# Performance work log

Hardware: AMD Instinct MI355X
Metric: run time of the kernel (lower is better)

## Reference

```python
import jax, jax.numpy as jnp
import numpy as np

B, N, C, K = 8, 2048, 512, 1


def setup_inputs() -> dict:
    key = jax.random.key(0)
    ks = jax.random.split(key, 10)
    s = 1.0 / np.sqrt(C)
    f32 = jnp.float32
    return {
        "x": jax.random.normal(ks[0], (B, N, C), f32),
        "neighbors": jax.random.randint(ks[1], (N, K), 0, N),
        "Wq": jax.random.normal(ks[2], (C, C), f32) * s,
        "bq": jnp.zeros((C,), f32),
        "Wk": jax.random.normal(ks[3], (C, C), f32) * s,
        "bk": jnp.zeros((C,), f32),
        "Wv": jax.random.normal(ks[4], (C, C), f32) * s,
        "bv": jnp.zeros((C,), f32),
        "rel_bias": jnp.zeros((K, K), f32),  # nn.Parameter(torch.zeros(k,k))
        "Wo": jax.random.normal(ks[5], (C, C), f32) * s,
        "bo": jnp.zeros((C,), f32),
    }


def reference(x, neighbors, Wq, bq, Wk, bk, Wv, bv, rel_bias, Wo, bo):
    # torch Linear: y = x @ W.T + b
    Q = jnp.einsum("bnc,dc->bnd", x, Wq) + bq
    Kt = jnp.einsum("bnc,dc->bnd", x, Wk) + bk
    V = jnp.einsum("bnc,dc->bnd", x, Wv) + bv

    nbr = neighbors[:, 0]  # [N], the single neighbor of each position (k==1)
    Kn = Kt[:, nbr, :]     # [B,N,C] gathered keys
    Vn = V[:, nbr, :]      # [B,N,C] gathered values (V_neighbors viewed as [B,N,k*C])

    # per-position score q_i . k_{nbr_i} + bias scalar
    s = jnp.einsum("bnc,bnc->bn", Q, Kn) + rel_bias[0, 0]

    # dense NxN score matrix, zeros elsewhere (faithful: softmax includes the zeros)
    scores = jnp.zeros((B, N, N), x.dtype).at[:, jnp.arange(N), nbr].set(s)
    probs = jax.nn.softmax(scores / jnp.asarray(np.sqrt(C), x.dtype), axis=-1)

    out = jnp.einsum("bnm,bmc->bnc", probs, Vn)
    return jnp.einsum("bnc,dc->bnd", out, Wo) + bo
```

## Files before the change

### kernel.cpp

```cpp
#include <hip/hip_runtime.h>
#include <hip/hip_bf16.h>
#include <math.h>

namespace {
constexpr int kB = 8;
constexpr int kN = 2048;
constexpr int kC = 512;
constexpr int kR = kB * kN;
constexpr int kNC = 2 * kC;
constexpr float kInvSqrtC = 0.044194173824159216f;

typedef __attribute__((ext_vector_type(8))) short short8;
typedef __attribute__((ext_vector_type(4))) short short4b;
typedef __attribute__((ext_vector_type(4))) float f32x4;
typedef unsigned short ushort;
}

static __device__ __forceinline__ float bf2f(ushort u) {
  union { unsigned int i; float f; } v; v.i = (unsigned int)u << 16; return v.f;
}
static __device__ __forceinline__ ushort f2bf(float f) {
  __hip_bfloat16 h = __float2bfloat16(f);
  union { __hip_bfloat16 h; ushort u; } cv; cv.h = h; return cv.u;
}

#define GLOAD16(G, L) __builtin_amdgcn_global_load_lds( \
    (const __attribute__((address_space(1))) unsigned int*)(G), \
    (__attribute__((address_space(3))) unsigned int*)(L), 16, 0, 0)

__global__ __launch_bounds__(256) void castw_kernel(
    const float* __restrict__ Wq, const float* __restrict__ Wk,
    const float* __restrict__ Wv, const float* __restrict__ Wo,
    ushort* __restrict__ WqT, ushort* __restrict__ WkT,
    ushort* __restrict__ WvT, ushort* __restrict__ Woh,
    const int* __restrict__ nbr, int* __restrict__ cnt) {
  const int z = blockIdx.z;
  const int t = threadIdx.x;
  if (z == 4) {
    if (blockIdx.x || blockIdx.y) return;
    __shared__ int h[kN];
#pragma unroll
    for (int i = 0; i < 8; i++) h[t + i * 256] = 0;
    __syncthreads();
#pragma unroll
    for (int i = 0; i < 8; i++) atomicAdd(&h[nbr[t + i * 256]], 1);
    __syncthreads();
#pragma unroll
    for (int i = 0; i < 8; i++) cnt[t + i * 256] = h[t + i * 256];
    return;
  }
  const int d0 = blockIdx.x * 64, c0 = blockIdx.y * 64;
  if (z == 3) {
#pragma unroll
    for (int i = 0; i < 4; i++) {
      const int row = i * 16 + (t >> 4), col4 = (t & 15) * 4;
      const float4 v = *reinterpret_cast<const float4*>(&Wo[(d0 + row) * kC + c0 + col4]);
      short4b o;
      o[0] = (short)f2bf(v.x); o[1] = (short)f2bf(v.y);
      o[2] = (short)f2bf(v.z); o[3] = (short)f2bf(v.w);
      *reinterpret_cast<short4b*>(&Woh[(d0 + row) * kC + c0 + col4]) = o;
    }
    return;
  }
  __shared__ float ld[64][65];
  const float* S = (z == 0) ? Wq : ((z == 1) ? Wk : Wv);
  ushort* T = (z == 0) ? WqT : ((z == 1) ? WkT : WvT);
#pragma unroll
  for (int i = 0; i < 4; i++) {
    const int dl = i * 16 + (t >> 4), cl4 = (t & 15) * 4;
    const float4 v = *reinterpret_cast<const float4*>(&S[(d0 + dl) * kC + c0 + cl4]);
    ld[dl][cl4 + 0] = v.x; ld[dl][cl4 + 1] = v.y;
    ld[dl][cl4 + 2] = v.z; ld[dl][cl4 + 3] = v.w;
  }
  __syncthreads();
#pragma unroll
  for (int i = 0; i < 4; i++) {
    const int cl = i * 16 + (t >> 4), dl4 = (t & 15) * 4;
    short4b o;
#pragma unroll
    for (int q = 0; q < 4; q++) o[q] = (short)f2bf(ld[dl4 + q][cl]);
    *reinterpret_cast<short4b*>(&T[(size_t)(c0 + cl) * kC + d0 + dl4]) = o;
  }
}

__global__ __launch_bounds__(256) void fold_kernel(
    const ushort* __restrict__ WqT, const ushort* __restrict__ WkT,
    const ushort* __restrict__ Woh, const ushort* __restrict__ WvT,
    ushort* __restrict__ Bh,
    const float* __restrict__ bq, const float* __restrict__ bk, const float* __restrict__ bv,
    float* __restrict__ biascat, float* __restrict__ vbq, float* __restrict__ bqbk) {
  const int t = threadIdx.x, lane = t & 63, w = t >> 6;
  const int z = blockIdx.z;
  if (z == 2) {
    const int fid = blockIdx.y * 8 + blockIdx.x;
    const int gw = fid * 4 + w;
    for (int rr = gw; rr < 1536; rr += 256) {
      const ushort* rowp; const float* vec;
      if (rr < 512)       { rowp = &WqT[(size_t)rr * kC];          vec = bk; }
      else if (rr < 1024) { rowp = &WkT[(size_t)(rr - 512) * kC];  vec = bq; }
      else                { rowp = &Woh[(size_t)(rr - 1024) * kC]; vec = bv; }
      const short8 u = *reinterpret_cast<const short8*>(&rowp[lane * 8]);
      const float4 v0 = *reinterpret_cast<const float4*>(&vec[lane * 8]);
      const float4 v1 = *reinterpret_cast<const float4*>(&vec[lane * 8 + 4]);
      float a = bf2f((ushort)u[0]) * v0.x + bf2f((ushort)u[1]) * v0.y +
                bf2f((ushort)u[2]) * v0.z + bf2f((ushort)u[3]) * v0.w +
                bf2f((ushort)u[4]) * v1.x + bf2f((ushort)u[5]) * v1.y +
                bf2f((ushort)u[6]) * v1.z + bf2f((ushort)u[7]) * v1.w;
#pragma unroll
      for (int off = 32; off; off >>= 1) a += __shfl_xor(a, off);
      if (lane == 0) {
        if (rr < 512) biascat[rr] = a;
        else if (rr < 1024) vbq[rr - 512] = a;
        else biascat[rr - 512] = a;
      }
    }
    if (gw == 0) {
      const float4 q0 = *reinterpret_cast<const float4*>(&bq[lane * 8]);
      const float4 q1 = *reinterpret_cast<const float4*>(&bq[lane * 8 + 4]);
      const float4 k0 = *reinterpret_cast<const float4*>(&bk[lane * 8]);
      const float4 k1 = *reinterpret_cast<const float4*>(&bk[lane * 8 + 4]);
      float s = q0.x * k0.x + q0.y * k0.y + q0.z * k0.z + q0.w * k0.w +
                q1.x * k1.x + q1.y * k1.y + q1.z * k1.z + q1.w * k1.w;
#pragma unroll
      for (int off = 32; off; off >>= 1) s += __shfl_xor(s, off);
      if (lane == 0) bqbk[0] = s;
    }
    return;
  }
  __shared__ ushort lA[64 * 64];
  __shared__ ushort lB[64 * 64];
  const ushort* Ap = z ? Woh : WqT;
  const ushort* Bp = z ? WvT : WkT;
  const int r0 = blockIdx.y * 64, c0 = blockIdx.x * 64;
  const int wr = (w >> 1) * 32, wc = (w & 1) * 32;
  const int srow = t >> 3, scol = (t & 7) * 8;
  f32x4 acc[2][2] = {};
  for (int k0 = 0; k0 < kC; k0 += 64) {
#pragma unroll
    for (int it = 0; it < 2; it++) {
      GLOAD16(&Ap[(size_t)(r0 + it * 32 + srow) * kC + k0 + scol], &lA[(it * 32 + srow) * 64 + scol]);
      GLOAD16(&Bp[(size_t)(c0 + it * 32 + srow) * kC + k0 + scol], &lB[(it * 32 + srow) * 64 + scol]);
    }
    __syncthreads();
#pragma unroll
    for (int kk = 0; kk < 2; kk++) {
      const int ko = kk * 32 + (lane >> 4) * 8;
      short8 af[2], bfr[2];
#pragma unroll
      for (int i = 0; i < 2; i++)
        af[i] = *reinterpret_cast<const short8*>(&lA[(wr + i * 16 + (lane & 15)) * 64 + ko]);
#pragma unroll
      for (int j = 0; j < 2; j++)
        bfr[j] = *reinterpret_cast<const short8*>(&lB[(wc + j * 16 + (lane & 15)) * 64 + ko]);
#pragma unroll
      for (int i = 0; i < 2; i++)
#pragma unroll
        for (int j = 0; j < 2; j++)
          acc[i][j] = __builtin_amdgcn_mfma_f32_16x16x32_bf16(af[i], bfr[j], acc[i][j], 0, 0, 0);
    }
    __syncthreads();
  }
#pragma unroll
  for (int j = 0; j < 2; j++) {
    const int col = c0 + wc + j * 16 + (lane & 15);
#pragma unroll
    for (int i = 0; i < 2; i++) {
      const int rbase = r0 + wr + i * 16 + (lane >> 4) * 4;
#pragma unroll
      for (int q = 0; q < 4; q++)
        Bh[(size_t)(z * kC + rbase + q) * kC + col] = f2bf(acc[i][j][q]);
    }
  }
}

__global__ __launch_bounds__(256) void castg_kernel(
    const float* __restrict__ x, const float* __restrict__ vbq,
    ushort* __restrict__ xh, float* __restrict__ g) {
  const int wid = threadIdx.x >> 6, lane = threadIdx.x & 63;
  const int r = blockIdx.x * 4 + wid;
  const float4 a = *reinterpret_cast<const float4*>(&x[(size_t)r * kC + lane * 8]);
  const float4 b = *reinterpret_cast<const float4*>(&x[(size_t)r * kC + lane * 8 + 4]);
  short8 o;
  o[0] = (short)f2bf(a.x); o[1] = (short)f2bf(a.y);
  o[2] = (short)f2bf(a.z); o[3] = (short)f2bf(a.w);
  o[4] = (short)f2bf(b.x); o[5] = (short)f2bf(b.y);
  o[6] = (short)f2bf(b.z); o[7] = (short)f2bf(b.w);
  *reinterpret_cast<short8*>(&xh[(size_t)r * kC + lane * 8]) = o;
  const float4 v0 = *reinterpret_cast<const float4*>(&vbq[lane * 8]);
  const float4 v1 = *reinterpret_cast<const float4*>(&vbq[lane * 8 + 4]);
  float acc = a.x * v0.x + a.y * v0.y + a.z * v0.z + a.w * v0.w +
              b.x * v1.x + b.y * v1.y + b.z * v1.z + b.w * v1.w;
#pragma unroll
  for (int off = 32; off; off >>= 1) acc += __shfl_xor(acc, off);
  if (lane == 0) g[r] = acc;
}

__global__ __launch_bounds__(256) void mm_kernel(
    const ushort* __restrict__ xh, const ushort* __restrict__ Bh,
    const float* __restrict__ biascat, const int* __restrict__ cnt,
    ushort* __restrict__ obuf, float* __restrict__ part2) {
  __shared__ ushort lA[2][128 * 64];
  __shared__ ushort lB[2][128 * 64];
  __shared__ float cs[2][128];
  const int id = blockIdx.x;
  const int orig = (id & 7) * 128 + (id >> 3);
  const int r0 = (orig >> 3) * 128;
  const int c0 = (orig & 7) * 128;
  const int t = threadIdx.x;
  const int lane = t & 63, w = t >> 6;
  const int wr = (w >> 1) * 64, wc = (w & 1) * 64;
  const int srow = t >> 3, scol = (t & 7) * 8;
  f32x4 acc[4][4] = {};

  auto stage = [&](int buf, int k0) {
#pragma unroll
    for (int it = 0; it < 4; it++) {
      GLOAD16(&xh[(size_t)(r0 + it * 32 + srow) * kC + k0 + scol],
              &lA[buf][(it * 32 + srow) * 64 + scol]);
      GLOAD16(&Bh[(size_t)(c0 + it * 32 + srow) * kC + k0 + scol],
              &lB[buf][(it * 32 + srow) * 64 + scol]);
    }
  };

  stage(0, 0);
  __syncthreads();
  int cur = 0;
#pragma unroll
  for (int ts = 0; ts < 8; ++ts) {
    if (ts < 7) stage(cur ^ 1, (ts + 1) * 64);
#pragma unroll
    for (int kk = 0; kk < 2; kk++) {
      const int ko = kk * 32 + (lane >> 4) * 8;
      short8 af[4], bfr[4];
#pragma unroll
      for (int i = 0; i < 4; i++)
        af[i] = *reinterpret_cast<const short8*>(&lA[cur][(wr + i * 16 + (lane & 15)) * 64 + ko]);
#pragma unroll
      for (int j = 0; j < 4; j++)
        bfr[j] = *reinterpret_cast<const short8*>(&lB[cur][(wc + j * 16 + (lane & 15)) * 64 + ko]);
      __builtin_amdgcn_s_setprio(1);
#pragma unroll
      for (int i = 0; i < 4; i++)
#pragma unroll
        for (int j = 0; j < 4; j++)
          acc[i][j] = __builtin_amdgcn_mfma_f32_16x16x32_bf16(af[i], bfr[j], acc[i][j], 0, 0, 0);
      __builtin_amdgcn_s_setprio(0);
    }
    __syncthreads();
    cur ^= 1;
  }

  const bool isVo = (c0 >= 512);
  float cw[4][4];
  if (isVo) {
    const int jb0 = (r0 & (kN - 1)) + wr + ((lane >> 4) << 2);
#pragma unroll
    for (int i = 0; i < 4; i++) {
      const int4 c4 = *reinterpret_cast<const int4*>(&cnt[jb0 + i * 16]);
      cw[i][0] = (float)c4.x; cw[i][1] = (float)c4.y;
      cw[i][2] = (float)c4.z; cw[i][3] = (float)c4.w;
    }
  }
  float psum[4] = {0.f, 0.f, 0.f, 0.f};
#pragma unroll
  for (int j = 0; j < 4; j++) {
    const int col = c0 + wc + j * 16 + (lane & 15);
    const float bias = biascat[col];
#pragma unroll
    for (int i = 0; i < 4; i++) {
      const int rbase = r0 + wr + i * 16 + (lane >> 4) * 4;
#pragma unroll
      for (int q = 0; q < 4; q++) {
        const float v = acc[i][j][q] + bias;
        obuf[(size_t)(rbase + q) * kNC + col] = f2bf(v);
        if (isVo) psum[j] += v * cw[i][q];
      }
    }
  }
  if (isVo) {
#pragma unroll
    for (int j = 0; j < 4; j++) {
      psum[j] += __shfl_xor(psum[j], 16);
      psum[j] += __shfl_xor(psum[j], 32);
    }
    if (lane < 16) {
#pragma unroll
      for (int j = 0; j < 4; j++) cs[w >> 1][wc + j * 16 + lane] = psum[j];
    }
    __syncthreads();
    if (t < 128) {
      const int b = r0 >> 11, rt = (r0 & (kN - 1)) >> 7;
      part2[(size_t)(b * 16 + rt) * kC + (c0 - 512) + t] = cs[0][t] + cs[1][t];
    }
  }
}

__global__ __launch_bounds__(256) void svo_reduce_kernel(
    const float* __restrict__ part2, float* __restrict__ svo) {
  const int d = blockIdx.x * 256 + threadIdx.x;
  const int b = blockIdx.y;
  float a = 0.f;
#pragma unroll
  for (int rt = 0; rt < 16; rt++) a += part2[(size_t)(b * 16 + rt) * kC + d];
  svo[b * kC + d] = a;
}

__global__ __launch_bounds__(256) void final_kernel(
    const ushort* __restrict__ xh, const ushort* __restrict__ obuf,
    const float* __restrict__ svo, const float* __restrict__ g, const int* __restrict__ nbr,
    const float* __restrict__ bqbk, const float* __restrict__ rb, const float* __restrict__ bo,
    float* __restrict__ out) {
  const int wid = threadIdx.x >> 6, lane = threadIdx.x & 63;
  const int rg = blockIdx.x * 4 + wid;
  const int b = rg >> 11, n = rg & (kN - 1);
  const int j = nbr[n];
  const int j2 = nbr[j];
  const short8 xv = *reinterpret_cast<const short8*>(&xh[(size_t)rg * kC + lane * 8]);
  const short8 wv = *reinterpret_cast<const short8*>(&obuf[(size_t)(b * kN + j) * kNC + lane * 8]);
  float a = 0.f;
#pragma unroll
  for (int q = 0; q < 8; q++) a += bf2f((ushort)xv[q]) * bf2f((ushort)wv[q]);
#pragma unroll
  for (int off = 32; off; off >>= 1) a += __shfl_xor(a, off);
  const float s = a + g[b * kN + j] + bqbk[0] + rb[0];
  const float tt = s * kInvSqrtC;
  const float e = expf(tt);
  const float inv = 1.0f / (e + (float)(kN - 1));
  const float coef = (e - 1.0f) * inv;
  const short8 vv = *reinterpret_cast<const short8*>(&obuf[(size_t)(b * kN + j2) * kNC + kC + lane * 8]);
  const float4 s0 = *reinterpret_cast<const float4*>(&svo[b * kC + lane * 8]);
  const float4 s1 = *reinterpret_cast<const float4*>(&svo[b * kC + lane * 8 + 4]);
  const float4 b0 = *reinterpret_cast<const float4*>(&bo[lane * 8]);
  const float4 b1 = *reinterpret_cast<const float4*>(&bo[lane * 8 + 4]);
  float4 r0, r1;
  r0.x = s0.x * inv + bf2f((ushort)vv[0]) * coef + b0.x;
  r0.y = s0.y * inv + bf2f((ushort)vv[1]) * coef + b0.y;
  r0.z = s0.z * inv + bf2f((ushort)vv[2]) * coef + b0.z;
  r0.w = s0.w * inv + bf2f((ushort)vv[3]) * coef + b0.w;
  r1.x = s1.x * inv + bf2f((ushort)vv[4]) * coef + b1.x;
  r1.y = s1.y * inv + bf2f((ushort)vv[5]) * coef + b1.y;
  r1.z = s1.z * inv + bf2f((ushort)vv[6]) * coef + b1.z;
  r1.w = s1.w * inv + bf2f((ushort)vv[7]) * coef + b1.w;
  *reinterpret_cast<float4*>(&out[(size_t)rg * kC + lane * 8]) = r0;
  *reinterpret_cast<float4*>(&out[(size_t)rg * kC + lane * 8 + 4]) = r1;
}

extern "C" void kernel_launch(void* const* d_in, const int* in_sizes, int n_in,
                              void* d_out, int out_size, void* d_ws, size_t ws_size,
                              hipStream_t stream) {
  const float* x  = (const float*)d_in[0];
  const int* nbr  = (const int*)d_in[1];
  const float* Wq = (const float*)d_in[2];
  const float* bq = (const float*)d_in[3];
  const float* Wk = (const float*)d_in[4];
  const float* bk = (const float*)d_in[5];
  const float* Wv = (const float*)d_in[6];
  const float* bv = (const float*)d_in[7];
  const float* rb = (const float*)d_in[8];
  const float* Wo = (const float*)d_in[9];
  const float* bo = (const float*)d_in[10];
  float* out = (float*)d_out;

  char* ws = (char*)d_ws;
  size_t off = 0;
  auto alloc = [&](size_t bytes) -> void* {
    void* p = ws + off;
    off = (off + bytes + 255) & ~(size_t)255;
    return p;
  };
  ushort* xh    = (ushort*)alloc((size_t)kR * kC * 2);
  ushort* Bh    = (ushort*)alloc((size_t)kNC * kC * 2);
  ushort* obuf  = (ushort*)alloc((size_t)kR * kNC * 2);
  ushort* WqT   = (ushort*)alloc((size_t)kC * kC * 2);
  ushort* WkT   = (ushort*)alloc((size_t)kC * kC * 2);
  ushort* WvT   = (ushort*)alloc((size_t)kC * kC * 2);
  ushort* Woh   = (ushort*)alloc((size_t)kC * kC * 2);
  float* biascat = (float*)alloc(kNC * 4);
  float* vbq    = (float*)alloc(kC * 4);
  float* bqbk   = (float*)alloc(4);
  int*   cnt    = (int*)alloc(kN * 4);
  float* g      = (float*)alloc((size_t)kR * 4);
  float* svo    = (float*)alloc((size_t)kB * kC * 4);
  float* part2  = (float*)alloc((size_t)kB * 16 * kC * 4);
  (void)ws_size; (void)n_in; (void)in_sizes; (void)out_size;

  castw_kernel<<<dim3(8, 8, 5), 256, 0, stream>>>(Wq, Wk, Wv, Wo, WqT, WkT, WvT, Woh, nbr, cnt);
  fold_kernel<<<dim3(8, 8, 3), 256, 0, stream>>>(WqT, WkT, Woh, WvT, Bh, bq, bk, bv, biascat, vbq, bqbk);
  castg_kernel<<<kR / 4, 256, 0, stream>>>(x, vbq, xh, g);
  mm_kernel<<<1024, 256, 0, stream>>>(xh, Bh, biascat, cnt, obuf, part2);
  svo_reduce_kernel<<<dim3(2, kB), 256, 0, stream>>>(part2, svo);
  final_kernel<<<kR / 4, 256, 0, stream>>>(xh, obuf, svo, g, nbr, bqbk, rb, bo, out);
}
```

Before: 70.86 us.

## Merge x cast into prep kernel, stage GEMM epilogue through LDS, fuse aux reductions

The x-to-bf16 cast moves into the weight-prep launch as extra grid slices, so it can run before the weight fold. The g dot product is recomputed from bf16 xh inside a new aux kernel that also does the svo reduction, removing one launch. The mm epilogue now writes fp32 tiles to reused LDS and then emits coalesced 16-byte bf16 stores instead of scattered 2-byte stores. The cost is an extra LDS round trip and a barrier in the epilogue, and g now carries slightly lower precision because it is computed from bf16 inputs.

Result: slower. 72.36 us (+2.1%).

```diff
diff --git a/kernel.cpp b/kernel.cpp
--- a/kernel.cpp
+++ b/kernel.cpp
@@ -28,17 +28,33 @@
     (const __attribute__((address_space(1))) unsigned int*)(G), \
     (__attribute__((address_space(3))) unsigned int*)(L), 16, 0, 0)
 
-__global__ __launch_bounds__(256) void castw_kernel(
+__global__ __launch_bounds__(256) void prep_kernel(
     const float* __restrict__ Wq, const float* __restrict__ Wk,
     const float* __restrict__ Wv, const float* __restrict__ Wo,
     ushort* __restrict__ WqT, ushort* __restrict__ WkT,
     ushort* __restrict__ WvT, ushort* __restrict__ Woh,
-    const int* __restrict__ nbr, int* __restrict__ cnt) {
+    const int* __restrict__ nbr, int* __restrict__ cnt,
+    const float* __restrict__ x, ushort* __restrict__ xh) {
+  __shared__ __align__(16) char sm[64 * 65 * 4];
   const int z = blockIdx.z;
   const int t = threadIdx.x;
+  if (z >= 5) {
+    const int wid = t >> 6, lane = t & 63;
+    const int bid = blockIdx.y * 8 + blockIdx.x;
+    const int r = ((z - 5) * 64 + bid) * 4 + wid;
+    const float4 a = *reinterpret_cast<const float4*>(&x[(size_t)r * kC + lane * 8]);
+    const float4 b = *reinterpret_cast<const float4*>(&x[(size_t)r * kC + lane * 8 + 4]);
+    short8 o;
+    o[0] = (short)f2bf(a.x); o[1] = (short)f2bf(a.y);
+    o[2] = (short)f2bf(a.z); o[3] = (short)f2bf(a.w);
+    o[4] = (short)f2bf(b.x); o[5] = (short)f2bf(b.y);
+    o[6] = (short)f2bf(b.z); o[7] = (short)f2bf(b.w);
+    *reinterpret_cast<short8*>(&xh[(size_t)r * kC + lane * 8]) = o;
+    return;
+  }
   if (z == 4) {
     if (blockIdx.x || blockIdx.y) return;
-    __shared__ int h[kN];
+    int* h = (int*)sm;
 #pragma unroll
     for (int i = 0; i < 8; i++) h[t + i * 256] = 0;
     __syncthreads();
@@ -62,7 +78,7 @@
     }
     return;
   }
-  __shared__ float ld[64][65];
+  float (*ld)[65] = (float(*)[65])sm;
   const float* S = (z == 0) ? Wq : ((z == 1) ? Wk : Wv);
   ushort* T = (z == 0) ? WqT : ((z == 1) ? WkT : WvT);
 #pragma unroll
@@ -173,35 +189,14 @@
   }
 }
 
-__global__ __launch_bounds__(256) void castg_kernel(
-    const float* __restrict__ x, const float* __restrict__ vbq,
-    ushort* __restrict__ xh, float* __restrict__ g) {
-  const int wid = threadIdx.x >> 6, lane = threadIdx.x & 63;
-  const int r = blockIdx.x * 4 + wid;
-  const float4 a = *reinterpret_cast<const float4*>(&x[(size_t)r * kC + lane * 8]);
-  const float4 b = *reinterpret_cast<const float4*>(&x[(size_t)r * kC + lane * 8 + 4]);
-  short8 o;
-  o[0] = (short)f2bf(a.x); o[1] = (short)f2bf(a.y);
-  o[2] = (short)f2bf(a.z); o[3] = (short)f2bf(a.w);
-  o[4] = (short)f2bf(b.x); o[5] = (short)f2bf(b.y);
-  o[6] = (short)f2bf(b.z); o[7] = (short)f2bf(b.w);
-  *reinterpret_cast<short8*>(&xh[(size_t)r * kC + lane * 8]) = o;
-  const float4 v0 = *reinterpret_cast<const float4*>(&vbq[lane * 8]);
-  const float4 v1 = *reinterpret_cast<const float4*>(&vbq[lane * 8 + 4]);
-  float acc = a.x * v0.x + a.y * v0.y + a.z * v0.z + a.w * v0.w +
-              b.x * v1.x + b.y * v1.y + b.z * v1.z + b.w * v1.w;
-#pragma unroll
-  for (int off = 32; off; off >>= 1) acc += __shfl_xor(acc, off);
-  if (lane == 0) g[r] = acc;
-}
-
 __global__ __launch_bounds__(256) void mm_kernel(
     const ushort* __restrict__ xh, const ushort* __restrict__ Bh,
     const float* __restrict__ biascat, const int* __restrict__ cnt,
     ushort* __restrict__ obuf, float* __restrict__ part2) {
-  __shared__ ushort lA[2][128 * 64];
-  __shared__ ushort lB[2][128 * 64];
-  __shared__ float cs[2][128];
+  __shared__ __align__(16) char smem[68608];
+  ushort* lds = (ushort*)smem;
+  float* fbuf = (float*)smem;
+  float* cs = (float*)(smem + 67584);
   const int id = blockIdx.x;
   const int orig = (id & 7) * 128 + (id >> 3);
   const int r0 = (orig >> 3) * 128;
@@ -216,9 +211,9 @@
 #pragma unroll
     for (int it = 0; it < 4; it++) {
       GLOAD16(&xh[(size_t)(r0 + it * 32 + srow) * kC + k0 + scol],
-              &lA[buf][(it * 32 + srow) * 64 + scol]);
+              lds + buf * 8192 + (it * 32 + srow) * 64 + scol);
       GLOAD16(&Bh[(size_t)(c0 + it * 32 + srow) * kC + k0 + scol],
-              &lB[buf][(it * 32 + srow) * 64 + scol]);
+              lds + 16384 + buf * 8192 + (it * 32 + srow) * 64 + scol);
     }
   };
 
@@ -234,10 +229,10 @@
       short8 af[4], bfr[4];
 #pragma unroll
       for (int i = 0; i < 4; i++)
-        af[i] = *reinterpret_cast<const short8*>(&lA[cur][(wr + i * 16 + (lane & 15)) * 64 + ko]);
+        af[i] = *reinterpret_cast<const short8*>(&lds[cur * 8192 + (wr + i * 16 + (lane & 15)) * 64 + ko]);
 #pragma unroll
       for (int j = 0; j < 4; j++)
-        bfr[j] = *reinterpret_cast<const short8*>(&lB[cur][(wc + j * 16 + (lane & 15)) * 64 + ko]);
+        bfr[j] = *reinterpret_cast<const short8*>(&lds[16384 + cur * 8192 + (wc + j * 16 + (lane & 15)) * 64 + ko]);
       __builtin_amdgcn_s_setprio(1);
 #pragma unroll
       for (int i = 0; i < 4; i++)
@@ -261,18 +256,20 @@
       cw[i][2] = (float)c4.z; cw[i][3] = (float)c4.w;
     }
   }
+  float bias[4];
+#pragma unroll
+  for (int j = 0; j < 4; j++) bias[j] = biascat[c0 + wc + j * 16 + (lane & 15)];
   float psum[4] = {0.f, 0.f, 0.f, 0.f};
 #pragma unroll
   for (int j = 0; j < 4; j++) {
-    const int col = c0 + wc + j * 16 + (lane & 15);
-    const float bias = biascat[col];
+    const int lcol = wc + j * 16 + (lane & 15);
 #pragma unroll
     for (int i = 0; i < 4; i++) {
-      const int rbase = r0 + wr + i * 16 + (lane >> 4) * 4;
+      const int lrow = wr + i * 16 + (lane >> 4) * 4;
 #pragma unroll
       for (int q = 0; q < 4; q++) {
-        const float v = acc[i][j][q] + bias;
-        obuf[(size_t)(rbase + q) * kNC + col] = f2bf(v);
+        const float v = acc[i][j][q] + bias[j];
+        fbuf[(lrow + q) * 132 + lcol] = v;
         if (isVo) psum[j] += v * cw[i][q];
       }
     }
@@ -285,24 +282,56 @@
     }
     if (lane < 16) {
 #pragma unroll
-      for (int j = 0; j < 4; j++) cs[w >> 1][wc + j * 16 + lane] = psum[j];
-    }
-    __syncthreads();
-    if (t < 128) {
-      const int b = r0 >> 11, rt = (r0 & (kN - 1)) >> 7;
-      part2[(size_t)(b * 16 + rt) * kC + (c0 - 512) + t] = cs[0][t] + cs[1][t];
-    }
-  }
-}
-
-__global__ __launch_bounds__(256) void svo_reduce_kernel(
-    const float* __restrict__ part2, float* __restrict__ svo) {
-  const int d = blockIdx.x * 256 + threadIdx.x;
-  const int b = blockIdx.y;
-  float a = 0.f;
-#pragma unroll
-  for (int rt = 0; rt < 16; rt++) a += part2[(size_t)(b * 16 + rt) * kC + d];
-  svo[b * kC + d] = a;
+      for (int j = 0; j < 4; j++) cs[(w >> 1) * 128 + wc + j * 16 + lane] = psum[j];
+    }
+  }
+  __syncthreads();
+  {
+    const int rr = t >> 1, h = t & 1;
+    const size_t grow = (size_t)(r0 + rr);
+#pragma unroll
+    for (int s = 0; s < 8; s++) {
+      const float4 a4 = *reinterpret_cast<const float4*>(&fbuf[rr * 132 + h * 64 + s * 8]);
+      const float4 b4 = *reinterpret_cast<const float4*>(&fbuf[rr * 132 + h * 64 + s * 8 + 4]);
+      short8 o;
+      o[0] = (short)f2bf(a4.x); o[1] = (short)f2bf(a4.y);
+      o[2] = (short)f2bf(a4.z); o[3] = (short)f2bf(a4.w);
+      o[4] = (short)f2bf(b4.x); o[5] = (short)f2bf(b4.y);
+      o[6] = (short)f2bf(b4.z); o[7] = (short)f2bf(b4.w);
+      *reinterpret_cast<short8*>(&obuf[grow * kNC + c0 + h * 64 + s * 8]) = o;
+    }
+  }
+  if (isVo && t < 128) {
+    const int b = r0 >> 11, rt = (r0 & (kN - 1)) >> 7;
+    part2[(size_t)(b * 16 + rt) * kC + (c0 - 512) + t] = cs[t] + cs[128 + t];
+  }
+}
+
+__global__ __launch_bounds__(256) void aux_kernel(
+    const float* __restrict__ part2, float* __restrict__ svo,
+    const ushort* __restrict__ xh, const float* __restrict__ vbq, float* __restrict__ g) {
+  const int bx = blockIdx.x;
+  if (bx < 16) {
+    const int d = (bx & 1) * 256 + threadIdx.x;
+    const int b = bx >> 1;
+    float a = 0.f;
+#pragma unroll
+    for (int rt = 0; rt < 16; rt++) a += part2[(size_t)(b * 16 + rt) * kC + d];
+    svo[b * kC + d] = a;
+    return;
+  }
+  const int wid = threadIdx.x >> 6, lane = threadIdx.x & 63;
+  const int r = (bx - 16) * 4 + wid;
+  const short8 u = *reinterpret_cast<const short8*>(&xh[(size_t)r * kC + lane * 8]);
+  const float4 v0 = *reinterpret_cast<const float4*>(&vbq[lane * 8]);
+  const float4 v1 = *reinterpret_cast<const float4*>(&vbq[lane * 8 + 4]);
+  float a = bf2f((ushort)u[0]) * v0.x + bf2f((ushort)u[1]) * v0.y +
+            bf2f((ushort)u[2]) * v0.z + bf2f((ushort)u[3]) * v0.w +
+            bf2f((ushort)u[4]) * v1.x + bf2f((ushort)u[5]) * v1.y +
+            bf2f((ushort)u[6]) * v1.z + bf2f((ushort)u[7]) * v1.w;
+#pragma unroll
+  for (int off = 32; off; off >>= 1) a += __shfl_xor(a, off);
+  if (lane == 0) g[r] = a;
 }
 
 __global__ __launch_bounds__(256) void final_kernel(
@@ -384,10 +413,9 @@
   float* part2  = (float*)alloc((size_t)kB * 16 * kC * 4);
   (void)ws_size; (void)n_in; (void)in_sizes; (void)out_size;
 
-  castw_kernel<<<dim3(8, 8, 5), 256, 0, stream>>>(Wq, Wk, Wv, Wo, WqT, WkT, WvT, Woh, nbr, cnt);
+  prep_kernel<<<dim3(8, 8, 69), 256, 0, stream>>>(Wq, Wk, Wv, Wo, WqT, WkT, WvT, Woh, nbr, cnt, x, xh);
   fold_kernel<<<dim3(8, 8, 3), 256, 0, stream>>>(WqT, WkT, Woh, WvT, Bh, bq, bk, bv, biascat, vbq, bqbk);
-  castg_kernel<<<kR / 4, 256, 0, stream>>>(x, vbq, xh, g);
   mm_kernel<<<1024, 256, 0, stream>>>(xh, Bh, biascat, cnt, obuf, part2);
-  svo_reduce_kernel<<<dim3(2, kB), 256, 0, stream>>>(part2, svo);
+  aux_kernel<<<16 + kR / 4, 256, 0, stream>>>(part2, svo, xh, vbq, g);
   final_kernel<<<kR / 4, 256, 0, stream>>>(xh, obuf, svo, g, nbr, bqbk, rb, bo, out);
 }
```

## Compact GEMM rows to referenced neighbor positions and skip unused row tiles

Applied to the files above, without the earlier changes.

The neighbor histogram kernel now also builds a compacted list of positions that are referenced at least once, with their counts. The main GEMM gathers A rows through this list, scatters outputs back to the original rows, and exits early for row tiles beyond the compacted count (writing zero partial sums). With random neighbors only about 63% of positions are referenced, so roughly a third of GEMM tiles can be skipped. The cost is a serial-ish prefix scan in one block, indirect row loads and scattered stores. Rows of obuf that are never referenced are left unwritten, so correctness depends on final_kernel only reading referenced rows.

Measured after the change: 67.99 us, median of 2. 4.0% less time.

```diff
diff --git a/kernel.cpp b/kernel.cpp
--- a/kernel.cpp
+++ b/kernel.cpp
@@ -33,12 +33,14 @@
     const float* __restrict__ Wv, const float* __restrict__ Wo,
     ushort* __restrict__ WqT, ushort* __restrict__ WkT,
     ushort* __restrict__ WvT, ushort* __restrict__ Woh,
-    const int* __restrict__ nbr, int* __restrict__ cnt) {
+    const int* __restrict__ nbr, int* __restrict__ cnt,
+    int* __restrict__ jlist, int* __restrict__ cnt_c, int* __restrict__ meta) {
   const int z = blockIdx.z;
   const int t = threadIdx.x;
   if (z == 4) {
     if (blockIdx.x || blockIdx.y) return;
     __shared__ int h[kN];
+    __shared__ int wsum[256];
 #pragma unroll
     for (int i = 0; i < 8; i++) h[t + i * 256] = 0;
     __syncthreads();
@@ -47,6 +49,30 @@
     __syncthreads();
 #pragma unroll
     for (int i = 0; i < 8; i++) cnt[t + i * 256] = h[t + i * 256];
+    const int base = t * 8;
+    int lpre[8], lc = 0;
+#pragma unroll
+    for (int i = 0; i < 8; i++) { lpre[i] = lc; lc += (h[base + i] > 0) ? 1 : 0; }
+    wsum[t] = lc;
+    __syncthreads();
+    for (int off = 1; off < 256; off <<= 1) {
+      const int v = (t >= off) ? wsum[t - off] : 0;
+      __syncthreads();
+      wsum[t] += v;
+      __syncthreads();
+    }
+    const int excl = (t == 0) ? 0 : wsum[t - 1];
+    const int total = wsum[255];
+#pragma unroll
+    for (int i = 0; i < 8; i++) {
+      if (h[base + i] > 0) {
+        const int p = excl + lpre[i];
+        jlist[p] = base + i;
+        cnt_c[p] = h[base + i];
+      }
+    }
+    for (int p = total + t; p < kN; p += 256) { jlist[p] = 0; cnt_c[p] = 0; }
+    if (t == 0) meta[0] = total;
     return;
   }
   const int d0 = blockIdx.x * 64, c0 = blockIdx.y * 64;
@@ -197,25 +223,36 @@
 
 __global__ __launch_bounds__(256) void mm_kernel(
     const ushort* __restrict__ xh, const ushort* __restrict__ Bh,
-    const float* __restrict__ biascat, const int* __restrict__ cnt,
+    const float* __restrict__ biascat,
+    const int* __restrict__ cnt_c, const int* __restrict__ jlist, const int* __restrict__ meta,
     ushort* __restrict__ obuf, float* __restrict__ part2) {
   __shared__ ushort lA[2][128 * 64];
   __shared__ ushort lB[2][128 * 64];
   __shared__ float cs[2][128];
   const int id = blockIdx.x;
   const int orig = (id & 7) * 128 + (id >> 3);
-  const int r0 = (orig >> 3) * 128;
+  const int rt = orig >> 3;
   const int c0 = (orig & 7) * 128;
+  const int b = rt >> 4, lt = rt & 15;
   const int t = threadIdx.x;
+  const bool isVo = (c0 >= 512);
+  if (lt * 128 >= meta[0]) {
+    if (isVo && t < 128)
+      part2[(size_t)(b * 16 + lt) * kC + (c0 - 512) + t] = 0.f;
+    return;
+  }
   const int lane = t & 63, w = t >> 6;
   const int wr = (w >> 1) * 64, wc = (w & 1) * 64;
   const int srow = t >> 3, scol = (t & 7) * 8;
+  int jl[4];
+#pragma unroll
+  for (int it = 0; it < 4; it++) jl[it] = jlist[lt * 128 + it * 32 + srow];
   f32x4 acc[4][4] = {};
 
   auto stage = [&](int buf, int k0) {
 #pragma unroll
     for (int it = 0; it < 4; it++) {
-      GLOAD16(&xh[(size_t)(r0 + it * 32 + srow) * kC + k0 + scol],
+      GLOAD16(&xh[(size_t)(b * kN + jl[it]) * kC + k0 + scol],
               &lA[buf][(it * 32 + srow) * 64 + scol]);
       GLOAD16(&Bh[(size_t)(c0 + it * 32 + srow) * kC + k0 + scol],
               &lB[buf][(it * 32 + srow) * 64 + scol]);
@@ -250,13 +287,18 @@
     cur ^= 1;
   }
 
-  const bool isVo = (c0 >= 512);
+  const int cbase = lt * 128 + wr + ((lane >> 4) << 2);
   float cw[4][4];
+  int rj[4][4];
+#pragma unroll
+  for (int i = 0; i < 4; i++) {
+    const int4 j4 = *reinterpret_cast<const int4*>(&jlist[cbase + i * 16]);
+    rj[i][0] = j4.x; rj[i][1] = j4.y; rj[i][2] = j4.z; rj[i][3] = j4.w;
+  }
   if (isVo) {
-    const int jb0 = (r0 & (kN - 1)) + wr + ((lane >> 4) << 2);
 #pragma unroll
     for (int i = 0; i < 4; i++) {
-      const int4 c4 = *reinterpret_cast<const int4*>(&cnt[jb0 + i * 16]);
+      const int4 c4 = *reinterpret_cast<const int4*>(&cnt_c[cbase + i * 16]);
       cw[i][0] = (float)c4.x; cw[i][1] = (float)c4.y;
       cw[i][2] = (float)c4.z; cw[i][3] = (float)c4.w;
     }
@@ -268,11 +310,10 @@
     const float bias = biascat[col];
 #pragma unroll
     for (int i = 0; i < 4; i++) {
-      const int rbase = r0 + wr + i * 16 + (lane >> 4) * 4;
 #pragma unroll
       for (int q = 0; q < 4; q++) {
         const float v = acc[i][j][q] + bias;
-        obuf[(size_t)(rbase + q) * kNC + col] = f2bf(v);
+        obuf[(size_t)(b * kN + rj[i][q]) * kNC + col] = f2bf(v);
         if (isVo) psum[j] += v * cw[i][q];
       }
     }
@@ -289,8 +330,7 @@
     }
     __syncthreads();
     if (t < 128) {
-      const int b = r0 >> 11, rt = (r0 & (kN - 1)) >> 7;
-      part2[(size_t)(b * 16 + rt) * kC + (c0 - 512) + t] = cs[0][t] + cs[1][t];
+      part2[(size_t)(b * 16 + lt) * kC + (c0 - 512) + t] = cs[0][t] + cs[1][t];
     }
   }
 }
@@ -379,15 +419,19 @@
   float* vbq    = (float*)alloc(kC * 4);
   float* bqbk   = (float*)alloc(4);
   int*   cnt    = (int*)alloc(kN * 4);
+  int*   jlist  = (int*)alloc(kN * 4);
+  int*   cnt_c  = (int*)alloc(kN * 4);
+  int*   meta   = (int*)alloc(256);
   float* g      = (float*)alloc((size_t)kR * 4);
   float* svo    = (float*)alloc((size_t)kB * kC * 4);
   float* part2  = (float*)alloc((size_t)kB * 16 * kC * 4);
   (void)ws_size; (void)n_in; (void)in_sizes; (void)out_size;
 
-  castw_kernel<<<dim3(8, 8, 5), 256, 0, stream>>>(Wq, Wk, Wv, Wo, WqT, WkT, WvT, Woh, nbr, cnt);
+  castw_kernel<<<dim3(8, 8, 5), 256, 0, stream>>>(Wq, Wk, Wv, Wo, WqT, WkT, WvT, Woh,
+                                                  nbr, cnt, jlist, cnt_c, meta);
   fold_kernel<<<dim3(8, 8, 3), 256, 0, stream>>>(WqT, WkT, Woh, WvT, Bh, bq, bk, bv, biascat, vbq, bqbk);
   castg_kernel<<<kR / 4, 256, 0, stream>>>(x, vbq, xh, g);
-  mm_kernel<<<1024, 256, 0, stream>>>(xh, Bh, biascat, cnt, obuf, part2);
+  mm_kernel<<<1024, 256, 0, stream>>>(xh, Bh, biascat, cnt_c, jlist, meta, obuf, part2);
   svo_reduce_kernel<<<dim3(2, kB), 256, 0, stream>>>(part2, svo);
   final_kernel<<<kR / 4, 256, 0, stream>>>(xh, obuf, svo, g, nbr, bqbk, rb, bo, out);
 }
```
